# Kernel optimization log

Measured on AMD Instinct MI355X. Metric: run time of the kernel, lower is better.

The kernel has to match this reference:

```python
import jax, jax.numpy as jnp
import numpy as np

N_NODES = 100000
N_EDGES = 1600000
IN_DIM = 128
HEADS = 4
OUT_C = 32
NEG_SLOPE = 0.2


def setup_inputs() -> dict:
    key = jax.random.key(0)
    ks = jax.random.split(key, 8)
    x = jax.random.normal(ks[0], (N_NODES, IN_DIM), dtype=jnp.float32)
    # glorot-ish scale for linear weights
    s = float(np.sqrt(2.0 / (IN_DIM + HEADS * OUT_C)))
    W_l = jax.random.normal(ks[1], (IN_DIM, HEADS * OUT_C), dtype=jnp.float32) * s
    b_l = jnp.zeros((HEADS * OUT_C,), dtype=jnp.float32)
    W_r = jax.random.normal(ks[2], (IN_DIM, HEADS * OUT_C), dtype=jnp.float32) * s
    b_r = jnp.zeros((HEADS * OUT_C,), dtype=jnp.float32)
    att = jax.random.normal(ks[3], (HEADS, OUT_C), dtype=jnp.float32) * float(np.sqrt(2.0 / (HEADS + OUT_C)))
    bias = jnp.zeros((HEADS * OUT_C,), dtype=jnp.float32)
    src = jax.random.randint(ks[4], (N_EDGES,), 0, N_NODES, dtype=jnp.int64)
    dst = jax.random.randint(ks[5], (N_EDGES,), 0, N_NODES, dtype=jnp.int64)
    # remove accidental self loops (the module strips them before re-adding)
    dst = jnp.where(dst == src, (dst + 1) % N_NODES, dst)
    return {"x": x, "W_l": W_l, "b_l": b_l, "W_r": W_r, "b_r": b_r,
            "att": att, "bias": bias, "src": src, "dst": dst}


def reference(x, W_l, b_l, W_r, b_r, att, bias, src, dst):
    N = x.shape[0]
    H, C = att.shape
    # linear transforms: source (lin_l) and target (lin_r) projections
    x_l = (x @ W_l + b_l).reshape(N, H, C)
    x_r = (x @ W_r + b_r).reshape(N, H, C)
    # add self loops (static shape)
    loop = jnp.arange(N, dtype=src.dtype)
    s = jnp.concatenate([src, loop])
    d = jnp.concatenate([dst, loop])
    # per-edge GATv2 score: a^T LeakyReLU(Theta_l x_j + Theta_r x_i)
    m = x_l[s] + x_r[d]                       # [E+N, H, C]
    m = jnp.where(m >= 0, m, NEG_SLOPE * m)   # LeakyReLU
    e = jnp.einsum('ehc,hc->eh', m, att)      # [E+N, H]
    # scatter-softmax over incoming edges of each destination node
    seg_max = jax.ops.segment_max(e, d, num_segments=N)   # [N, H]
    e = jnp.exp(e - seg_max[d])
    denom = jax.ops.segment_sum(e, d, num_segments=N)     # [N, H]
    alpha = e / denom[d]                                   # every node has a self loop -> denom > 0
    # weighted scatter-add of source messages
    out = jax.ops.segment_sum(alpha[:, :, None] * x_l[s], d, num_segments=N)  # [N, H, C]
    return out.reshape(N, H * C) + bias
```

## Files before the change

### kernel.cpp

```cpp
#include <hip/hip_runtime.h>
#include <hip/hip_bf16.h>
#include <cstdint>

#define N_NODES 100000
#define N_EDGES 1600000
#define DIM 128
#define GR 32

__device__ __forceinline__ float lrelu(float v) { return v >= 0.f ? v : 0.2f * v; }

__global__ __launch_bounds__(256) void gemm_dual(
    const float* __restrict__ x,
    const float* __restrict__ Wl, const float* __restrict__ bl,
    const float* __restrict__ Wr, const float* __restrict__ br,
    float* __restrict__ xl, float* __restrict__ xr) {
  __shared__ float xs[GR][DIM];
  const int tid = threadIdx.x;
  const int row0 = blockIdx.x * GR;

#pragma unroll
  for (int i = 0; i < 4; ++i) {
    const int idx = i * 256 + tid;
    const int r = idx >> 5;
    const int c4 = idx & 31;
    const float4 v = *reinterpret_cast<const float4*>(
        x + (size_t)(row0 + r) * DIM + c4 * 4);
    *reinterpret_cast<float4*>(&xs[r][c4 * 4]) = v;
  }
  __syncthreads();

  const int cg = tid & 63;
  const int rg = tid >> 6;
  const int which = cg >> 5;
  const int col0 = (cg & 31) * 4;
  const float* __restrict__ W = which ? Wr : Wl;
  const float* __restrict__ b = which ? br : bl;
  float* __restrict__ o = which ? xr : xl;
  const int r0 = rg * 8;

  float acc[8][4];
#pragma unroll
  for (int r = 0; r < 8; ++r)
#pragma unroll
    for (int c = 0; c < 4; ++c) acc[r][c] = 0.f;

  for (int kb = 0; kb < DIM; kb += 4) {
    float4 w0 = *reinterpret_cast<const float4*>(W + (kb + 0) * DIM + col0);
    float4 w1 = *reinterpret_cast<const float4*>(W + (kb + 1) * DIM + col0);
    float4 w2 = *reinterpret_cast<const float4*>(W + (kb + 2) * DIM + col0);
    float4 w3 = *reinterpret_cast<const float4*>(W + (kb + 3) * DIM + col0);
#pragma unroll
    for (int r = 0; r < 8; ++r) {
      const float4 xv = *reinterpret_cast<const float4*>(&xs[r0 + r][kb]);
      acc[r][0] = fmaf(xv.x, w0.x, acc[r][0]);
      acc[r][1] = fmaf(xv.x, w0.y, acc[r][1]);
      acc[r][2] = fmaf(xv.x, w0.z, acc[r][2]);
      acc[r][3] = fmaf(xv.x, w0.w, acc[r][3]);
      acc[r][0] = fmaf(xv.y, w1.x, acc[r][0]);
      acc[r][1] = fmaf(xv.y, w1.y, acc[r][1]);
      acc[r][2] = fmaf(xv.y, w1.z, acc[r][2]);
      acc[r][3] = fmaf(xv.y, w1.w, acc[r][3]);
      acc[r][0] = fmaf(xv.z, w2.x, acc[r][0]);
      acc[r][1] = fmaf(xv.z, w2.y, acc[r][1]);
      acc[r][2] = fmaf(xv.z, w2.z, acc[r][2]);
      acc[r][3] = fmaf(xv.z, w2.w, acc[r][3]);
      acc[r][0] = fmaf(xv.w, w3.x, acc[r][0]);
      acc[r][1] = fmaf(xv.w, w3.y, acc[r][1]);
      acc[r][2] = fmaf(xv.w, w3.z, acc[r][2]);
      acc[r][3] = fmaf(xv.w, w3.w, acc[r][3]);
    }
  }

  const float4 bb = *reinterpret_cast<const float4*>(b + col0);
#pragma unroll
  for (int r = 0; r < 8; ++r) {
    float4 ov;
    ov.x = acc[r][0] + bb.x;
    ov.y = acc[r][1] + bb.y;
    ov.z = acc[r][2] + bb.z;
    ov.w = acc[r][3] + bb.w;
    *reinterpret_cast<float4*>(o + (size_t)(row0 + r0 + r) * DIM + col0) = ov;
  }
}

__global__ __launch_bounds__(256) void hist_kernel(const int* __restrict__ dst,
                                                   int* __restrict__ deg) {
  const int i = blockIdx.x * 256 + threadIdx.x;
  if (i < N_EDGES) atomicAdd(&deg[dst[i]], 1);
}

__global__ __launch_bounds__(1024) void scan1(const int* __restrict__ deg,
                                              int* __restrict__ excl,
                                              int* __restrict__ bsum) {
  __shared__ int tmp[1024];
  const int tid = threadIdx.x;
  const int gid = blockIdx.x * 1024 + tid;
  const int v = (gid < N_NODES) ? deg[gid] : 0;
  int xacc = v;
  tmp[tid] = v;
  __syncthreads();
  for (int offd = 1; offd < 1024; offd <<= 1) {
    const int t = (tid >= offd) ? tmp[tid - offd] : 0;
    __syncthreads();
    xacc += t;
    tmp[tid] = xacc;
    __syncthreads();
  }
  if (gid < N_NODES) excl[gid] = xacc - v;
  if (tid == 1023) bsum[blockIdx.x] = xacc;
}

__global__ __launch_bounds__(128) void scan2(int* __restrict__ bsum, int nb) {
  __shared__ int tmp[128];
  const int tid = threadIdx.x;
  const int v = (tid < nb) ? bsum[tid] : 0;
  int xacc = v;
  tmp[tid] = v;
  __syncthreads();
  for (int offd = 1; offd < 128; offd <<= 1) {
    const int t = (tid >= offd) ? tmp[tid - offd] : 0;
    __syncthreads();
    xacc += t;
    tmp[tid] = xacc;
    __syncthreads();
  }
  if (tid < nb) bsum[tid] = xacc - v;
}

__global__ __launch_bounds__(1024) void scan3(int* __restrict__ offs,
                                              const int* __restrict__ bsum,
                                              int* __restrict__ fill) {
  const int gid = blockIdx.x * 1024 + threadIdx.x;
  if (gid < N_NODES) {
    const int o = offs[gid] + bsum[blockIdx.x];
    offs[gid] = o;
    fill[gid] = o;
  }
  if (gid == N_NODES) offs[N_NODES] = N_EDGES;
}

__global__ __launch_bounds__(256) void scatter_kernel(const int* __restrict__ src,
                                                      const int* __restrict__ dst,
                                                      int* __restrict__ fill,
                                                      int* __restrict__ csr) {
  const int i = blockIdx.x * 256 + threadIdx.x;
  if (i < N_EDGES) {
    const int slot = atomicAdd(&fill[dst[i]], 1);
    csr[slot] = src[i];
  }
}

__global__ __launch_bounds__(256) void gat_node(
    const float* __restrict__ xl,
    const float* __restrict__ att, const float* __restrict__ bias,
    const int* __restrict__ offs, const int* __restrict__ csr,
    float* __restrict__ out) {
  const int wid = (blockIdx.x * 256 + threadIdx.x) >> 6;
  const int lane = threadIdx.x & 63;
  if (wid >= N_NODES) return;
  const int d = wid;

  const float2 a2 = reinterpret_cast<const float2*>(att)[lane];
  const float2 xr2 = reinterpret_cast<const float2*>(out + (size_t)d * DIM)[lane];
  const float2 xls = reinterpret_cast<const float2*>(xl + (size_t)d * DIM)[lane];

  float e = lrelu(xls.x + xr2.x) * a2.x + lrelu(xls.y + xr2.y) * a2.y;
  e += __shfl_xor(e, 1);
  e += __shfl_xor(e, 2);
  e += __shfl_xor(e, 4);
  e += __shfl_xor(e, 8);
  float mrun = e;
  float lrun = 1.f;
  float accx = xls.x, accy = xls.y;

  const int beg = offs[d];
  const int end = offs[d + 1];

  for (int cbase = beg; cbase < end; cbase += 64) {
    const int idx = cbase + lane;
    const int sv = csr[idx < end ? idx : end - 1];
    const int cnt = min(64, end - cbase);

    auto ldrow = [&](int j) -> float2 {
      const int s = __shfl(sv, j < cnt ? j : 0);
      return reinterpret_cast<const float2*>(xl + (size_t)s * DIM)[lane];
    };
    float2 A = ldrow(0);
    float2 B = ldrow(1);
    float2 C = ldrow(2);
    float2 D = ldrow(3);

    for (int j = 0; j < cnt; ++j) {
      const float2 xc = A;
      A = B; B = C; C = D;
      if (j + 4 < cnt) {
        const int s = __shfl(sv, j + 4);
        D = reinterpret_cast<const float2*>(xl + (size_t)s * DIM)[lane];
      }
      float ek = lrelu(xc.x + xr2.x) * a2.x + lrelu(xc.y + xr2.y) * a2.y;
      ek += __shfl_xor(ek, 1);
      ek += __shfl_xor(ek, 2);
      ek += __shfl_xor(ek, 4);
      ek += __shfl_xor(ek, 8);
      const float mn = fmaxf(mrun, ek);
      const float sc = __expf(mrun - mn);
      const float wgt = __expf(ek - mn);
      lrun = lrun * sc + wgt;
      accx = fmaf(wgt, xc.x, accx * sc);
      accy = fmaf(wgt, xc.y, accy * sc);
      mrun = mn;
    }
  }

  const float2 b2 = reinterpret_cast<const float2*>(bias)[lane];
  float2 o;
  o.x = accx / lrun + b2.x;
  o.y = accy / lrun + b2.y;
  reinterpret_cast<float2*>(out + (size_t)d * DIM)[lane] = o;
}

extern "C" void kernel_launch(void* const* d_in, const int* in_sizes, int n_in,
                              void* d_out, int out_size, void* d_ws, size_t ws_size,
                              hipStream_t stream) {
  const float* x    = (const float*)d_in[0];
  const float* Wl   = (const float*)d_in[1];
  const float* bl   = (const float*)d_in[2];
  const float* Wr   = (const float*)d_in[3];
  const float* br   = (const float*)d_in[4];
  const float* att  = (const float*)d_in[5];
  const float* bias = (const float*)d_in[6];
  const int* src    = (const int*)d_in[7];
  const int* dst    = (const int*)d_in[8];
  float* out = (float*)d_out;

  char* w = (char*)d_ws;
  size_t off = 0;
  auto alloc = [&](size_t bytes) -> void* {
    void* p = w + off;
    off = (off + bytes + 255) & ~(size_t)255;
    return p;
  };
  float* xl = (float*)alloc((size_t)N_NODES * DIM * 4);
  int* deg  = (int*)alloc((size_t)N_NODES * 4);
  int* offs = (int*)alloc((size_t)(N_NODES + 1) * 4);
  int* fill = (int*)alloc((size_t)N_NODES * 4);
  int* bsum = (int*)alloc(1024);
  int* csr  = (int*)alloc((size_t)N_EDGES * 4);
  float* xr = out;

  const int nscan_blocks = (N_NODES + 1023) / 1024;

  hipMemsetAsync(deg, 0, (size_t)N_NODES * 4, stream);
  gemm_dual<<<N_NODES / GR, 256, 0, stream>>>(x, Wl, bl, Wr, br, xl, xr);
  hist_kernel<<<(N_EDGES + 255) / 256, 256, 0, stream>>>(dst, deg);
  scan1<<<nscan_blocks, 1024, 0, stream>>>(deg, offs, bsum);
  scan2<<<1, 128, 0, stream>>>(bsum, nscan_blocks);
  scan3<<<nscan_blocks, 1024, 0, stream>>>(offs, bsum, fill);
  scatter_kernel<<<(N_EDGES + 255) / 256, 256, 0, stream>>>(src, dst, fill, csr);
  gat_node<<<(N_NODES * 64 + 255) / 256, 256, 0, stream>>>(xl, att, bias, offs, csr, out);
}
```

Measured before the change: 545.8 us.

## Split each node's edge list across two half-waves with float4 loads and merge

The node kernel now has each 32-lane half of the wavefront process half of a node's incoming edges. Each lane loads a float4 of the source row and keeps its own online-softmax state, so the wave's per-edge loop runs about half as many serial iterations with one fewer shuffle per reduction. The two halves' running max, sum and accumulators are combined with a cross-half shuffle at the end. This cuts the serial dependency chain per node at the cost of extra masking and a final merge step.

```diff
diff --git a/kernel.cpp b/kernel.cpp
--- a/kernel.cpp
+++ b/kernel.cpp
@@ -8,6 +8,7 @@
 #define GR 32
 
 __device__ __forceinline__ float lrelu(float v) { return v >= 0.f ? v : 0.2f * v; }
+__device__ __forceinline__ float lr(float v) { return fmaxf(v, 0.2f * v); }
 
 __global__ __launch_bounds__(256) void gemm_dual(
     const float* __restrict__ x,
@@ -159,19 +160,27 @@
   const int lane = threadIdx.x & 63;
   if (wid >= N_NODES) return;
   const int d = wid;
-
-  const float2 a2 = reinterpret_cast<const float2*>(att)[lane];
-  const float2 xr2 = reinterpret_cast<const float2*>(out + (size_t)d * DIM)[lane];
-  const float2 xls = reinterpret_cast<const float2*>(xl + (size_t)d * DIM)[lane];
-
-  float e = lrelu(xls.x + xr2.x) * a2.x + lrelu(xls.y + xr2.y) * a2.y;
-  e += __shfl_xor(e, 1);
-  e += __shfl_xor(e, 2);
-  e += __shfl_xor(e, 4);
-  e += __shfl_xor(e, 8);
-  float mrun = e;
-  float lrun = 1.f;
-  float accx = xls.x, accy = xls.y;
+  const int i = lane & 31;
+  const int c0 = i * 4;
+  const bool h0 = lane < 32;
+
+  const float4 a4  = *reinterpret_cast<const float4*>(att + c0);
+  const float4 xr4 = *reinterpret_cast<const float4*>(out + (size_t)d * DIM + c0);
+  const float4 xls = *reinterpret_cast<const float4*>(xl + (size_t)d * DIM + c0);
+
+  float p = lr(xls.x + xr4.x) * a4.x + lr(xls.y + xr4.y) * a4.y
+          + lr(xls.z + xr4.z) * a4.z + lr(xls.w + xr4.w) * a4.w;
+  p += __shfl_xor(p, 1);
+  p += __shfl_xor(p, 2);
+  p += __shfl_xor(p, 4);
+
+  float m = h0 ? p : -1e30f;
+  float l = h0 ? 1.f : 0.f;
+  float4 acc;
+  acc.x = h0 ? xls.x : 0.f;
+  acc.y = h0 ? xls.y : 0.f;
+  acc.z = h0 ? xls.z : 0.f;
+  acc.w = h0 ? xls.w : 0.f;
 
   const int beg = offs[d];
   const int end = offs[d + 1];
@@ -180,43 +189,66 @@
     const int idx = cbase + lane;
     const int sv = csr[idx < end ? idx : end - 1];
     const int cnt = min(64, end - cbase);
-
-    auto ldrow = [&](int j) -> float2 {
-      const int s = __shfl(sv, j < cnt ? j : 0);
-      return reinterpret_cast<const float2*>(xl + (size_t)s * DIM)[lane];
+    const int nh = (cnt + 1) >> 1;
+
+    auto fetch = [&](int j) -> float4 {
+      const int jj = j < nh ? j : nh - 1;
+      const int pos = h0 ? jj : nh + jj;
+      const int s = __shfl(sv, pos);
+      return *reinterpret_cast<const float4*>(xl + (size_t)s * DIM + c0);
     };
-    float2 A = ldrow(0);
-    float2 B = ldrow(1);
-    float2 C = ldrow(2);
-    float2 D = ldrow(3);
-
-    for (int j = 0; j < cnt; ++j) {
-      const float2 xc = A;
-      A = B; B = C; C = D;
-      if (j + 4 < cnt) {
-        const int s = __shfl(sv, j + 4);
-        D = reinterpret_cast<const float2*>(xl + (size_t)s * DIM)[lane];
-      }
-      float ek = lrelu(xc.x + xr2.x) * a2.x + lrelu(xc.y + xr2.y) * a2.y;
+    float4 A = fetch(0);
+    float4 B = fetch(1);
+    float4 C = fetch(2);
+
+    for (int j = 0; j < nh; ++j) {
+      const float4 xv = A;
+      A = B; B = C;
+      if (j + 3 < nh) C = fetch(j + 3);
+      const int e = h0 ? j : nh + j;
+      const bool valid = e < cnt;
+
+      float ek = lr(xv.x + xr4.x) * a4.x + lr(xv.y + xr4.y) * a4.y
+               + lr(xv.z + xr4.z) * a4.z + lr(xv.w + xr4.w) * a4.w;
       ek += __shfl_xor(ek, 1);
       ek += __shfl_xor(ek, 2);
       ek += __shfl_xor(ek, 4);
-      ek += __shfl_xor(ek, 8);
-      const float mn = fmaxf(mrun, ek);
-      const float sc = __expf(mrun - mn);
-      const float wgt = __expf(ek - mn);
-      lrun = lrun * sc + wgt;
-      accx = fmaf(wgt, xc.x, accx * sc);
-      accy = fmaf(wgt, xc.y, accy * sc);
-      mrun = mn;
+      ek = valid ? ek : -2e30f;
+
+      const float mn = fmaxf(m, ek);
+      const float sc = __expf(m - mn);
+      float w = __expf(ek - mn);
+      w = valid ? w : 0.f;
+      l = l * sc + w;
+      acc.x = fmaf(acc.x, sc, w * xv.x);
+      acc.y = fmaf(acc.y, sc, w * xv.y);
+      acc.z = fmaf(acc.z, sc, w * xv.z);
+      acc.w = fmaf(acc.w, sc, w * xv.w);
+      m = mn;
     }
   }
 
-  const float2 b2 = reinterpret_cast<const float2*>(bias)[lane];
-  float2 o;
-  o.x = accx / lrun + b2.x;
-  o.y = accy / lrun + b2.y;
-  reinterpret_cast<float2*>(out + (size_t)d * DIM)[lane] = o;
+  const float mo = __shfl_xor(m, 32);
+  const float lo_ = __shfl_xor(l, 32);
+  float4 ao;
+  ao.x = __shfl_xor(acc.x, 32);
+  ao.y = __shfl_xor(acc.y, 32);
+  ao.z = __shfl_xor(acc.z, 32);
+  ao.w = __shfl_xor(acc.w, 32);
+  const float ms = fmaxf(m, mo);
+  const float ws = __expf(m - ms);
+  const float wo = __expf(mo - ms);
+  const float lm = l * ws + lo_ * wo;
+
+  if (h0) {
+    const float4 b4 = *reinterpret_cast<const float4*>(bias + c0);
+    float4 o;
+    o.x = (acc.x * ws + ao.x * wo) / lm + b4.x;
+    o.y = (acc.y * ws + ao.y * wo) / lm + b4.y;
+    o.z = (acc.z * ws + ao.z * wo) / lm + b4.z;
+    o.w = (acc.w * ws + ao.w * wo) / lm + b4.w;
+    *reinterpret_cast<float4*>(out + (size_t)d * DIM + c0) = o;
+  }
 }
 
 extern "C" void kernel_launch(void* const* d_in, const int* in_sizes, int n_in,
```

After: 508.3 us. -6.9%, faster.

## Process four edges per wavefront in GAT aggregation and fuse histogram into GEMM launch

Applied to the files above, without the earlier changes.

The node aggregation kernel now splits each 64-lane wavefront into four 16-lane groups. Each group handles a different neighbor with 8 channels per lane loaded as float4 pairs, and the four partial online-softmax states are merged with cross-lane shuffles at the end. This cuts the serial per-edge loop length and shuffle-reduction depth by about four, and issues wider loads. Separately, the degree histogram runs as extra blocks of the GEMM kernel launch, which removes one launch and lets the atomics overlap with the GEMM. The cost is more registers, masking work for partial groups, and an extra merge step.

```diff
diff --git a/kernel.cpp b/kernel.cpp
--- a/kernel.cpp
+++ b/kernel.cpp
@@ -6,16 +6,26 @@
 #define N_EDGES 1600000
 #define DIM 128
 #define GR 32
-
-__device__ __forceinline__ float lrelu(float v) { return v >= 0.f ? v : 0.2f * v; }
-
-__global__ __launch_bounds__(256) void gemm_dual(
+#define GEMM_BLOCKS (N_NODES / GR)
+#define HIST_BLOCKS ((N_EDGES + 255) / 256)
+
+__device__ __forceinline__ float lr(float v) { return fmaxf(v, 0.2f * v); }
+
+__global__ __launch_bounds__(256) void gemm_hist(
     const float* __restrict__ x,
     const float* __restrict__ Wl, const float* __restrict__ bl,
     const float* __restrict__ Wr, const float* __restrict__ br,
-    float* __restrict__ xl, float* __restrict__ xr) {
+    float* __restrict__ xl, float* __restrict__ xr,
+    const int* __restrict__ dst, int* __restrict__ deg) {
   __shared__ float xs[GR][DIM];
   const int tid = threadIdx.x;
+
+  if (blockIdx.x >= GEMM_BLOCKS) {
+    const int i = (blockIdx.x - GEMM_BLOCKS) * 256 + tid;
+    if (i < N_EDGES) atomicAdd(&deg[dst[i]], 1);
+    return;
+  }
+
   const int row0 = blockIdx.x * GR;
 
 #pragma unroll
@@ -83,12 +93,6 @@
   }
 }
 
-__global__ __launch_bounds__(256) void hist_kernel(const int* __restrict__ dst,
-                                                   int* __restrict__ deg) {
-  const int i = blockIdx.x * 256 + threadIdx.x;
-  if (i < N_EDGES) atomicAdd(&deg[dst[i]], 1);
-}
-
 __global__ __launch_bounds__(1024) void scan1(const int* __restrict__ deg,
                                               int* __restrict__ excl,
                                               int* __restrict__ bsum) {
@@ -159,19 +163,32 @@
   const int lane = threadIdx.x & 63;
   if (wid >= N_NODES) return;
   const int d = wid;
-
-  const float2 a2 = reinterpret_cast<const float2*>(att)[lane];
-  const float2 xr2 = reinterpret_cast<const float2*>(out + (size_t)d * DIM)[lane];
-  const float2 xls = reinterpret_cast<const float2*>(xl + (size_t)d * DIM)[lane];
-
-  float e = lrelu(xls.x + xr2.x) * a2.x + lrelu(xls.y + xr2.y) * a2.y;
-  e += __shfl_xor(e, 1);
-  e += __shfl_xor(e, 2);
-  e += __shfl_xor(e, 4);
-  e += __shfl_xor(e, 8);
-  float mrun = e;
-  float lrun = 1.f;
-  float accx = xls.x, accy = xls.y;
+  const int q = lane >> 4;
+  const int i = lane & 15;
+  const int c0 = i * 8;
+
+  const float4 aA = *reinterpret_cast<const float4*>(att + c0);
+  const float4 aB = *reinterpret_cast<const float4*>(att + c0 + 4);
+  const float4 rA = *reinterpret_cast<const float4*>(out + (size_t)d * DIM + c0);
+  const float4 rB = *reinterpret_cast<const float4*>(out + (size_t)d * DIM + c0 + 4);
+  const float4 sA = *reinterpret_cast<const float4*>(xl + (size_t)d * DIM + c0);
+  const float4 sB = *reinterpret_cast<const float4*>(xl + (size_t)d * DIM + c0 + 4);
+
+  float p = lr(sA.x + rA.x) * aA.x + lr(sA.y + rA.y) * aA.y
+          + lr(sA.z + rA.z) * aA.z + lr(sA.w + rA.w) * aA.w
+          + lr(sB.x + rB.x) * aB.x + lr(sB.y + rB.y) * aB.y
+          + lr(sB.z + rB.z) * aB.z + lr(sB.w + rB.w) * aB.w;
+  p += __shfl_xor(p, 1);
+  p += __shfl_xor(p, 2);
+
+  const bool q0 = (q == 0);
+  float m = q0 ? p : -1e30f;
+  float l = q0 ? 1.f : 0.f;
+  float4 cA, cB;
+  cA.x = q0 ? sA.x : 0.f;  cA.y = q0 ? sA.y : 0.f;
+  cA.z = q0 ? sA.z : 0.f;  cA.w = q0 ? sA.w : 0.f;
+  cB.x = q0 ? sB.x : 0.f;  cB.y = q0 ? sB.y : 0.f;
+  cB.z = q0 ? sB.z : 0.f;  cB.w = q0 ? sB.w : 0.f;
 
   const int beg = offs[d];
   const int end = offs[d + 1];
@@ -180,43 +197,82 @@
     const int idx = cbase + lane;
     const int sv = csr[idx < end ? idx : end - 1];
     const int cnt = min(64, end - cbase);
-
-    auto ldrow = [&](int j) -> float2 {
-      const int s = __shfl(sv, j < cnt ? j : 0);
-      return reinterpret_cast<const float2*>(xl + (size_t)s * DIM)[lane];
-    };
-    float2 A = ldrow(0);
-    float2 B = ldrow(1);
-    float2 C = ldrow(2);
-    float2 D = ldrow(3);
-
-    for (int j = 0; j < cnt; ++j) {
-      const float2 xc = A;
-      A = B; B = C; C = D;
-      if (j + 4 < cnt) {
-        const int s = __shfl(sv, j + 4);
-        D = reinterpret_cast<const float2*>(xl + (size_t)s * DIM)[lane];
+    const int nj = (cnt + 3) >> 2;
+
+    const int s0 = __shfl(sv, q);
+    const float* rp0 = xl + (size_t)s0 * DIM + c0;
+    float4 nA = *reinterpret_cast<const float4*>(rp0);
+    float4 nB = *reinterpret_cast<const float4*>(rp0 + 4);
+
+    for (int j = 0; j < nj; ++j) {
+      const float4 xA = nA;
+      const float4 xB = nB;
+      if (j + 1 < nj) {
+        const int s1 = __shfl(sv, 4 * (j + 1) + q);
+        const float* rp = xl + (size_t)s1 * DIM + c0;
+        nA = *reinterpret_cast<const float4*>(rp);
+        nB = *reinterpret_cast<const float4*>(rp + 4);
       }
-      float ek = lrelu(xc.x + xr2.x) * a2.x + lrelu(xc.y + xr2.y) * a2.y;
+      const bool valid = (4 * j + q) < cnt;
+
+      float ek = lr(xA.x + rA.x) * aA.x + lr(xA.y + rA.y) * aA.y
+               + lr(xA.z + rA.z) * aA.z + lr(xA.w + rA.w) * aA.w
+               + lr(xB.x + rB.x) * aB.x + lr(xB.y + rB.y) * aB.y
+               + lr(xB.z + rB.z) * aB.z + lr(xB.w + rB.w) * aB.w;
       ek += __shfl_xor(ek, 1);
       ek += __shfl_xor(ek, 2);
-      ek += __shfl_xor(ek, 4);
-      ek += __shfl_xor(ek, 8);
-      const float mn = fmaxf(mrun, ek);
-      const float sc = __expf(mrun - mn);
-      const float wgt = __expf(ek - mn);
-      lrun = lrun * sc + wgt;
-      accx = fmaf(wgt, xc.x, accx * sc);
-      accy = fmaf(wgt, xc.y, accy * sc);
-      mrun = mn;
+      ek = valid ? ek : -2e30f;
+
+      const float mn = fmaxf(m, ek);
+      const float sc = __expf(m - mn);
+      float w = __expf(ek - mn);
+      w = valid ? w : 0.f;
+      l = l * sc + w;
+      cA.x = fmaf(cA.x, sc, w * xA.x);
+      cA.y = fmaf(cA.y, sc, w * xA.y);
+      cA.z = fmaf(cA.z, sc, w * xA.z);
+      cA.w = fmaf(cA.w, sc, w * xA.w);
+      cB.x = fmaf(cB.x, sc, w * xB.x);
+      cB.y = fmaf(cB.y, sc, w * xB.y);
+      cB.z = fmaf(cB.z, sc, w * xB.z);
+      cB.w = fmaf(cB.w, sc, w * xB.w);
+      m = mn;
     }
   }
 
-  const float2 b2 = reinterpret_cast<const float2*>(bias)[lane];
-  float2 o;
-  o.x = accx / lrun + b2.x;
-  o.y = accy / lrun + b2.y;
-  reinterpret_cast<float2*>(out + (size_t)d * DIM)[lane] = o;
+  auto merge = [&](int mask) {
+    const float mo = __shfl_xor(m, mask);
+    const float lo = __shfl_xor(l, mask);
+    float4 oA, oB;
+    oA.x = __shfl_xor(cA.x, mask);  oA.y = __shfl_xor(cA.y, mask);
+    oA.z = __shfl_xor(cA.z, mask);  oA.w = __shfl_xor(cA.w, mask);
+    oB.x = __shfl_xor(cB.x, mask);  oB.y = __shfl_xor(cB.y, mask);
+    oB.z = __shfl_xor(cB.z, mask);  oB.w = __shfl_xor(cB.w, mask);
+    const float ms = fmaxf(m, mo);
+    const float w1 = __expf(m - ms);
+    const float w2 = __expf(mo - ms);
+    l = l * w1 + lo * w2;
+    cA.x = cA.x * w1 + oA.x * w2;  cA.y = cA.y * w1 + oA.y * w2;
+    cA.z = cA.z * w1 + oA.z * w2;  cA.w = cA.w * w1 + oA.w * w2;
+    cB.x = cB.x * w1 + oB.x * w2;  cB.y = cB.y * w1 + oB.y * w2;
+    cB.z = cB.z * w1 + oB.z * w2;  cB.w = cB.w * w1 + oB.w * w2;
+    m = ms;
+  };
+  merge(16);
+  merge(32);
+
+  if (lane < 16) {
+    const float inv = 1.f / l;
+    const float4 bA = *reinterpret_cast<const float4*>(bias + c0);
+    const float4 bB = *reinterpret_cast<const float4*>(bias + c0 + 4);
+    float4 oA, oB;
+    oA.x = cA.x * inv + bA.x;  oA.y = cA.y * inv + bA.y;
+    oA.z = cA.z * inv + bA.z;  oA.w = cA.w * inv + bA.w;
+    oB.x = cB.x * inv + bB.x;  oB.y = cB.y * inv + bB.y;
+    oB.z = cB.z * inv + bB.z;  oB.w = cB.w * inv + bB.w;
+    *reinterpret_cast<float4*>(out + (size_t)d * DIM + c0) = oA;
+    *reinterpret_cast<float4*>(out + (size_t)d * DIM + c0 + 4) = oB;
+  }
 }
 
 extern "C" void kernel_launch(void* const* d_in, const int* in_sizes, int n_in,
@@ -251,8 +307,8 @@
   const int nscan_blocks = (N_NODES + 1023) / 1024;
 
   hipMemsetAsync(deg, 0, (size_t)N_NODES * 4, stream);
-  gemm_dual<<<N_NODES / GR, 256, 0, stream>>>(x, Wl, bl, Wr, br, xl, xr);
-  hist_kernel<<<(N_EDGES + 255) / 256, 256, 0, stream>>>(dst, deg);
+  gemm_hist<<<GEMM_BLOCKS + HIST_BLOCKS, 256, 0, stream>>>(
+      x, Wl, bl, Wr, br, xl, xr, dst, deg);
   scan1<<<nscan_blocks, 1024, 0, stream>>>(deg, offs, bsum);
   scan2<<<1, 128, 0, stream>>>(bsum, nscan_blocks);
   scan3<<<nscan_blocks, 1024, 0, stream>>>(offs, bsum, fill);
```

Result: faster. 487.8 us (-10.6%).
